# Kernel tuning notes

Hardware: AMD Instinct MI355X
Metric: run time of the kernel (lower is better)

Reference implementation:

```python
import jax, jax.numpy as jnp
import numpy as np

ALPHA, GAMMA = 0.25, 2.0            # focal loss params (cfg defaults)
W_CLASS, W_BBOX, W_GIOU = 2.0, 5.0, 2.0
N_CANDIDATE_K = 5                   # top-k ious used to derive dynamic k
CENTER_RADIUS = 2.5
B, Q, G, C = 32, 2000, 64, 80
IMG_W, IMG_H = 1333.0, 800.0


def _box_iou(a, b):
    # a: [Q,4] xyxy, b: [G,4] xyxy -> iou [Q,G], union [Q,G]
    area_a = (a[:, 2] - a[:, 0]) * (a[:, 3] - a[:, 1])
    area_b = (b[:, 2] - b[:, 0]) * (b[:, 3] - b[:, 1])
    lt = jnp.maximum(a[:, None, :2], b[None, :, :2])
    rb = jnp.minimum(a[:, None, 2:], b[None, :, 2:])
    wh = jnp.clip(rb - lt, 0.0)
    inter = wh[..., 0] * wh[..., 1]
    union = area_a[:, None] + area_b[None, :] - inter
    return inter / union, union


def _generalized_box_iou(a, b):
    iou, union = _box_iou(a, b)
    lt = jnp.minimum(a[:, None, :2], b[None, :, :2])
    rb = jnp.maximum(a[:, None, 2:], b[None, :, 2:])
    wh = jnp.clip(rb - lt, 0.0)
    area_c = wh[..., 0] * wh[..., 1]
    return iou - (area_c - union) / area_c


def _get_in_boxes_info(boxes, gt):
    # boxes, gt: absolute xyxy. Anchor centers inside gt box / inside center region.
    cx = (boxes[:, 0] + boxes[:, 2]) * 0.5
    cy = (boxes[:, 1] + boxes[:, 3]) * 0.5
    is_in_boxes = ((cx[:, None] > gt[None, :, 0]) & (cx[:, None] < gt[None, :, 2]) &
                   (cy[:, None] > gt[None, :, 1]) & (cy[:, None] < gt[None, :, 3]))
    gt_cx = (gt[:, 0] + gt[:, 2]) * 0.5
    gt_cy = (gt[:, 1] + gt[:, 3]) * 0.5
    gt_w = gt[:, 2] - gt[:, 0]
    gt_h = gt[:, 3] - gt[:, 1]
    is_in_centers = ((cx[:, None] > (gt_cx - CENTER_RADIUS * gt_w)[None, :]) &
                     (cx[:, None] < (gt_cx + CENTER_RADIUS * gt_w)[None, :]) &
                     (cy[:, None] > (gt_cy - CENTER_RADIUS * gt_h)[None, :]) &
                     (cy[:, None] < (gt_cy + CENTER_RADIUS * gt_h)[None, :]))
    fg_mask = is_in_boxes.any(1) | is_in_centers.any(1)
    return fg_mask, is_in_boxes & is_in_centers


def _dedup(cost, matching):
    # queries matched to >1 gt keep only their min-cost gt
    over = matching.sum(1) > 1
    keep = jax.nn.one_hot(jnp.argmin(cost, axis=1), cost.shape[1], dtype=matching.dtype)
    return jnp.where(over[:, None], keep, matching)


def _dynamic_k_matching(cost, ious):
    Qn, Gn = cost.shape
    topk_ious = jax.lax.top_k(ious.T, N_CANDIDATE_K)[0]              # [G,k]
    dynamic_ks = jnp.maximum(topk_ious.sum(1).astype(jnp.int32), 1)  # [G]
    # rank of each query within each gt's cost column (ascending)
    ranks = jnp.argsort(jnp.argsort(cost, axis=0), axis=0)
    matching = (ranks < dynamic_ks[None, :]).astype(cost.dtype)      # [Q,G]
    matching = _dedup(cost, matching)

    # ensure every gt gets >=1 query; bounded loop replaces data-dependent while
    def body(_, carry):
        cost_c, match_c = carry
        unmatched = match_c.sum(0) == 0                              # [G]
        any_un = unmatched.any()
        matched_q = match_c.sum(1) > 0
        cost_n = cost_c + jnp.where(matched_q, 1e5, 0.0)[:, None]
        add = jax.nn.one_hot(jnp.argmin(cost_n, axis=0), Qn, dtype=match_c.dtype).T
        match_n = jnp.maximum(match_c, add * unmatched[None, :].astype(match_c.dtype))
        match_n = _dedup(cost_n, match_n)
        return (jnp.where(any_un, cost_n, cost_c), jnp.where(any_un, match_n, match_c))

    cost, matching = jax.lax.fori_loop(0, Gn, body, (cost, matching))
    masked = jnp.where(matching > 0, cost, jnp.inf)
    matched_query_id = jnp.argmin(masked, axis=0)                    # [G]
    return matching, matched_query_id


def _match_one(logits, boxes, tgt_ids, gt_boxes, size_out, size_tgt):
    fg_mask, in_bc = _get_in_boxes_info(boxes, gt_boxes)
    ious, _ = _box_iou(boxes, gt_boxes)                              # [Q,G]
    neg = (1.0 - ALPHA) * logits ** GAMMA * (-jnp.log(1.0 - logits + 1e-8))
    pos = ALPHA * (1.0 - logits) ** GAMMA * (-jnp.log(logits + 1e-8))
    cost_class = jnp.take(pos - neg, tgt_ids, axis=1)                # [Q,G]
    out_n = boxes / size_out                                         # [Q,4]
    tgt_n = gt_boxes / size_tgt                                      # [G,4]
    cost_bbox = jnp.abs(out_n[:, None, :] - tgt_n[None, :, :]).sum(-1)  # L1 cdist
    cost_giou = -_generalized_box_iou(boxes, gt_boxes)
    cost = (W_BBOX * cost_bbox + W_CLASS * cost_class + W_GIOU * cost_giou
            + 100.0 * (~in_bc).astype(cost_bbox.dtype))
    cost = cost + jnp.where(fg_mask, 0.0, 1e4)[:, None]
    return _dynamic_k_matching(cost, ious)


def _rand_boxes(key, n_shape):
    k1, k2 = jax.random.split(key)
    wh = jnp.array([IMG_W, IMG_H], jnp.float32)
    ctr = jax.random.uniform(k1, n_shape + (2,)) * wh
    size = jax.random.uniform(k2, n_shape + (2,)) * (wh * 0.3) + 8.0
    x1y1 = jnp.clip(ctr - size * 0.5, 0.0, wh)
    x2y2 = jnp.clip(ctr + size * 0.5, 0.0, wh)
    x2y2 = jnp.maximum(x2y2, x1y1 + 1.0)
    return jnp.concatenate([x1y1, x2y2], axis=-1)


def setup_inputs() -> dict:
    key = jax.random.key(0)
    k1, k2, k3, k4 = jax.random.split(key, 4)
    pred_logits = jax.random.uniform(k1, (B, Q, C), minval=1e-4, maxval=1.0 - 1e-4)
    pred_boxes = _rand_boxes(k2, (B, Q))
    gt_classes = jax.random.randint(k3, (B, G), 0, C)
    gt_boxes = _rand_boxes(k4, (B, G))
    sz = jnp.array([IMG_W, IMG_H, IMG_W, IMG_H], jnp.float32)
    return {
        'pred_logits': pred_logits,
        'pred_boxes': pred_boxes,
        'gt_classes': gt_classes,
        'gt_boxes': gt_boxes,
        'image_size_xyxy': jnp.tile(sz, (B, 1)),
        'image_size_xyxy_tgt': jnp.tile(sz, (B, G, 1)),
    }


def reference(pred_logits, pred_boxes, gt_classes, gt_boxes, image_size_xyxy, image_size_xyxy_tgt):
    # matching: [B,Q,G] 0/1 assignment matrix (row q matched to gt g);
    # matched_query_id: [B,G] best query per gt. Padded-G, fixed-shape analog of
    # the per-image variable-length (indices, matched_ids) lists.
    matching, matched_query_id = jax.vmap(_match_one)(
        pred_logits, pred_boxes, gt_classes, gt_boxes, image_size_xyxy, image_size_xyxy_tgt)
    return matching, matched_query_id
```

## Files before the change

### kernel.cpp

```cpp
#include <hip/hip_runtime.h>
#include <cmath>

#pragma clang fp contract(off)

#define BB 32
#define QQ 2000
#define GG 64
#define CCH 80
#define TOPC 16

__global__ __launch_bounds__(256) void cost_kernel(
    const float* __restrict__ logits, const float* __restrict__ boxes,
    const int* __restrict__ gtc, const float* __restrict__ gtb,
    const float* __restrict__ szout, const float* __restrict__ sztgt,
    float* __restrict__ cost, int* __restrict__ rowarg) {
#pragma clang fp contract(off)
  const int b = blockIdx.y;
  const int q0 = blockIdx.x * 64;
  const int t = threadIdx.x;
  const int w = t >> 6, lane = t & 63;

  __shared__ float4 s_qb[64];
  __shared__ float s_tile[64 * 65];

  const int gbase = (b * GG + lane) * 4;
  const float g0 = gtb[gbase + 0], g1 = gtb[gbase + 1];
  const float g2 = gtb[gbase + 2], g3 = gtb[gbase + 3];
  const float t0 = g0 / sztgt[gbase + 0], t1 = g1 / sztgt[gbase + 1];
  const float t2 = g2 / sztgt[gbase + 2], t3 = g3 / sztgt[gbase + 3];
  const float garea = (g2 - g0) * (g3 - g1);
  const float gcx = (g0 + g2) * 0.5f, gcy = (g1 + g3) * 0.5f;
  const float gw = g2 - g0, gh = g3 - g1;
  const float cxlo = gcx - 2.5f * gw, cxhi = gcx + 2.5f * gw;
  const float cylo = gcy - 2.5f * gh, cyhi = gcy + 2.5f * gh;
  const int cls = gtc[b * GG + lane];
  const float so0 = szout[b * 4 + 0], so1 = szout[b * 4 + 1];
  const float so2 = szout[b * 4 + 2], so3 = szout[b * 4 + 3];

  if (t < 64) {
    int q = q0 + t;
    s_qb[t] = (q < QQ) ? reinterpret_cast<const float4*>(boxes)[b * QQ + q]
                       : make_float4(0.f, 0.f, 1.f, 1.f);
  }
  __syncthreads();

  const float* lbase = logits + (size_t)b * QQ * CCH;
  for (int i = 0; i < 16; ++i) {
    const int qi = w * 16 + i;
    const int q = q0 + qi;
    float4 bx = s_qb[qi];
    float x1 = bx.x, y1 = bx.y, x2 = bx.z, y2 = bx.w;
    float on0 = x1 / so0, on1 = y1 / so1, on2 = x2 / so2, on3 = y2 / so3;
    float cx = (x1 + x2) * 0.5f, cy = (y1 + y2) * 0.5f;
    float areaa = (x2 - x1) * (y2 - y1);

    bool ib = (cx > g0) & (cx < g2) & (cy > g1) & (cy < g3);
    bool ic = (cx > cxlo) & (cx < cxhi) & (cy > cylo) & (cy < cyhi);
    bool fg = (__ballot(ib) != 0ull) || (__ballot(ic) != 0ull);
    float fgadd = fg ? 0.0f : 1e4f;

    float ltx = fmaxf(x1, g0), lty = fmaxf(y1, g1);
    float rbx = fminf(x2, g2), rby = fminf(y2, g3);
    float iw = fmaxf(rbx - ltx, 0.0f), ih = fmaxf(rby - lty, 0.0f);
    float inter = iw * ih;
    float uni = (areaa + garea) - inter;
    float iou = inter / uni;
    float ex1 = fminf(x1, g0), ey1 = fminf(y1, g1);
    float ex2 = fmaxf(x2, g2), ey2 = fmaxf(y2, g3);
    float ew = fmaxf(ex2 - ex1, 0.0f), eh = fmaxf(ey2 - ey1, 0.0f);
    float areac = ew * eh;
    float giou = iou - (areac - uni) / areac;

    float p = (q < QQ) ? lbase[(size_t)q * CCH + cls] : 0.5f;
    float negc = (0.75f * (p * p)) * (-logf((1.0f - p) + 1e-8f));
    float posc = (0.25f * ((1.0f - p) * (1.0f - p))) * (-logf(p + 1e-8f));
    float ccls = posc - negc;

    float cb = ((fabsf(on0 - t0) + fabsf(on1 - t1)) + fabsf(on2 - t2)) + fabsf(on3 - t3);
    float notbc = (ib & ic) ? 0.0f : 1.0f;
    float c = ((5.0f * cb + 2.0f * ccls) + 2.0f * (-giou)) + 100.0f * notbc;
    c = c + fgadd;

    s_tile[qi * 65 + lane] = c;

    float bv = c; int bg = lane;
    for (int off = 32; off; off >>= 1) {
      float ov = __shfl_down(bv, off, 64); int og = __shfl_down(bg, off, 64);
      if (ov < bv || (ov == bv && og < bg)) { bv = ov; bg = og; }
    }
    if (lane == 0 && q < QQ) rowarg[b * QQ + q] = bg;
  }
  __syncthreads();

  float* cb_out = cost + (size_t)b * GG * QQ;
  const int qi = t & 63;
  const int q = q0 + qi;
  if (q < QQ) {
    #pragma unroll
    for (int pass = 0; pass < 16; ++pass) {
      int g = (t >> 6) + pass * 4;
      cb_out[(size_t)g * QQ + q] = s_tile[qi * 65 + g];
    }
  }
}

__global__ __launch_bounds__(256) void pick_kernel(
    const float* __restrict__ boxes, const float* __restrict__ gtb,
    const float* __restrict__ cost, short* __restrict__ lists,
    int* __restrict__ dynks) {
#pragma clang fp contract(off)
  const int gwave = blockIdx.x * 4 + (threadIdx.x >> 6);
  const int lane = threadIdx.x & 63;
  const int b = gwave >> 6, col = gwave & 63;

  const int gbase = (b * GG + col) * 4;
  const float gx1 = gtb[gbase + 0], gy1 = gtb[gbase + 1];
  const float gx2 = gtb[gbase + 2], gy2 = gtb[gbase + 3];
  const float ga = (gx2 - gx1) * (gy2 - gy1);

  float v[32];
  #pragma unroll
  for (int j = 0; j < 32; ++j) {
    int q = lane + (j << 6);
    if (q < QQ) {
      float4 bx = reinterpret_cast<const float4*>(boxes)[b * QQ + q];
      float areaa = (bx.z - bx.x) * (bx.w - bx.y);
      float ltx = fmaxf(bx.x, gx1), lty = fmaxf(bx.y, gy1);
      float rbx = fminf(bx.z, gx2), rby = fminf(bx.w, gy2);
      float iw = fmaxf(rbx - ltx, 0.0f), ih = fmaxf(rby - lty, 0.0f);
      float inter = iw * ih;
      v[j] = inter / ((areaa + ga) - inter);
    } else v[j] = -1.0f;
  }
  unsigned rm = 0u;
  float s = 0.0f;
  for (int pass = 0; pass < 5; ++pass) {
    float bv = -1e30f; int bq = 0x7fffffff;
    #pragma unroll
    for (int j = 0; j < 32; ++j) {
      int q = lane + (j << 6);
      if (q < QQ && !((rm >> j) & 1u) && v[j] > bv) { bv = v[j]; bq = q; }
    }
    for (int off = 32; off; off >>= 1) {
      float ov = __shfl_down(bv, off, 64); int oq = __shfl_down(bq, off, 64);
      if (ov > bv || (ov == bv && oq < bq)) { bv = ov; bq = oq; }
    }
    bv = __shfl(bv, 0, 64); bq = __shfl(bq, 0, 64);
    s += bv;
    if ((bq & 63) == lane) rm |= (1u << (bq >> 6));
  }
  int dynk = (int)s;
  if (dynk < 1) dynk = 1;
  if (lane == 0) dynks[b * GG + col] = dynk;

  const float* ccol = cost + (size_t)(b * GG + col) * QQ;
  #pragma unroll
  for (int j = 0; j < 32; ++j) {
    int q = lane + (j << 6);
    v[j] = (q < QQ) ? ccol[q] : 0.0f;
  }
  rm = 0u;
  for (int pass = 0; pass < TOPC; ++pass) {
    float bv = INFINITY; int bq = 0x7fffffff;
    #pragma unroll
    for (int j = 0; j < 32; ++j) {
      int q = lane + (j << 6);
      if (q < QQ && !((rm >> j) & 1u) && v[j] < bv) { bv = v[j]; bq = q; }
    }
    for (int off = 32; off; off >>= 1) {
      float ov = __shfl_down(bv, off, 64); int oq = __shfl_down(bq, off, 64);
      if (ov < bv || (ov == bv && oq < bq)) { bv = ov; bq = oq; }
    }
    bq = __shfl(bq, 0, 64);
    if (lane == 0) lists[(b * GG + col) * TOPC + pass] = (short)bq;
    if ((bq & 63) == lane) rm |= (1u << (bq >> 6));
  }
}

__global__ __launch_bounds__(256) void serial_kernel(
    const float* __restrict__ cost, const short* __restrict__ lists,
    const int* __restrict__ dynks, const int* __restrict__ rowarg,
    uint2* __restrict__ bits, float* __restrict__ out_ids) {
#pragma clang fp contract(off)
  const int b = blockIdx.x;
  const int tid = threadIdx.x;
  const int w = tid >> 6, lane = tid & 63;

  __shared__ unsigned s_mlo[QQ], s_mhi[QQ];
  __shared__ int s_first[QQ];
  __shared__ int s_pushed[QQ];
  __shared__ short s_rarg[QQ];
  __shared__ short s_list[GG * TOPC];
  __shared__ int s_cnt[GG];
  __shared__ short s_chosen[GG];
  __shared__ unsigned long long s_pack[GG];
  __shared__ int s_added[128];
  __shared__ unsigned s_gmlo, s_gmhi;
  __shared__ int s_anyun, s_nadd;

  for (int q = tid; q < QQ; q += 256) {
    s_mlo[q] = 0u; s_mhi[q] = 0u; s_first[q] = -1; s_pushed[q] = -1;
    s_rarg[q] = (short)rowarg[b * QQ + q];
  }
  for (int i = tid; i < GG * TOPC; i += 256) s_list[i] = lists[b * GG * TOPC + i];
  if (tid < GG) s_cnt[tid] = 0;
  __syncthreads();

  if (tid < GG) {
    int dynk = dynks[b * GG + tid];
    s_cnt[tid] = dynk;
    for (int i = 0; i < dynk; ++i) {
      int q = s_list[tid * TOPC + i];
      if (tid < 32) atomicOr(&s_mlo[q], 1u << tid);
      else          atomicOr(&s_mhi[q], 1u << (tid - 32));
      s_first[q] = 0;
    }
  }
  __syncthreads();

  for (int q = tid; q < QQ; q += 256) {
    unsigned lo = s_mlo[q], hi = s_mhi[q];
    if (__popc(lo) + __popc(hi) > 1) {
      int bg = s_rarg[q];
      unsigned tl = lo, th = hi;
      while (tl) { int g = __ffs(tl) - 1; tl &= tl - 1; if (g != bg) atomicSub(&s_cnt[g], 1); }
      while (th) { int g = __ffs(th) + 31; th &= th - 1; if (g != bg) atomicSub(&s_cnt[g], 1); }
      bool had = (bg < 32) ? ((lo >> bg) & 1u) : ((hi >> (bg - 32)) & 1u);
      if (!had) atomicAdd(&s_cnt[bg], 1);
      s_mlo[q] = (bg < 32) ? (1u << bg) : 0u;
      s_mhi[q] = (bg >= 32) ? (1u << (bg - 32)) : 0u;
    }
  }

  const float* costb = cost + (size_t)b * GG * QQ;
  int T = 0;
  for (int iter = 0; iter < GG; ++iter) {
    __syncthreads();
    if (tid < 64) {
      unsigned long long bal = __ballot(s_cnt[tid] > 0);
      if (tid == 0) {
        s_gmlo = (unsigned)bal; s_gmhi = (unsigned)(bal >> 32);
        s_anyun = ((~bal) != 0ull); s_nadd = 0;
      }
    }
    __syncthreads();
    if (!s_anyun) break;
    T++;
    const unsigned gmlo = s_gmlo, gmhi = s_gmhi;

    for (int col = w; col < GG; col += 4) {
      bool matched = (col < 32) ? ((gmlo >> col) & 1u) : ((gmhi >> (col - 32)) & 1u);
      if (matched) continue;
      int cq = s_list[col * TOPC + (lane & (TOPC - 1))];
      bool cand_un = (lane < TOPC) && ((s_mlo[cq] | s_mhi[cq]) == 0u);
      unsigned long long bal = __ballot(cand_un);
      int q;
      if (bal) {
        q = s_list[col * TOPC + (__ffsll(bal) - 1)];
      } else {
        const float* ccol = costb + (size_t)col * QQ;
        float bv = INFINITY; int bq = 0x7fffffff;
        for (int q2 = lane; q2 < QQ; q2 += 64) {
          if ((s_mlo[q2] | s_mhi[q2]) == 0u) {
            float cv = ccol[q2];
            if (cv < bv) { bv = cv; bq = q2; }
          }
        }
        for (int off = 32; off; off >>= 1) {
          float ov = __shfl_down(bv, off, 64); int oq = __shfl_down(bq, off, 64);
          if (ov < bv || (ov == bv && oq < bq)) { bv = ov; bq = oq; }
        }
        bq = __shfl(bq, 0, 64);
        if (bq == 0x7fffffff) {
          bv = INFINITY; bq = 0x7fffffff;
          for (int q2 = lane; q2 < QQ; q2 += 64) {
            float cv = ccol[q2];
            int k = (s_first[q2] >= 0) ? (iter + 1 - s_first[q2]) : 0;
            for (int tt = 0; tt < k; ++tt) cv += 1e5f;
            if (cv < bv) { bv = cv; bq = q2; }
          }
          for (int off = 32; off; off >>= 1) {
            float ov = __shfl_down(bv, off, 64); int oq = __shfl_down(bq, off, 64);
            if (ov < bv || (ov == bv && oq < bq)) { bv = ov; bq = oq; }
          }
          bq = __shfl(bq, 0, 64);
        }
        q = bq;
      }
      if (lane == 0) s_chosen[col] = (short)q;
    }
    __syncthreads();

    if (tid < 64) {
      bool matched = (tid < 32) ? ((gmlo >> tid) & 1u) : ((gmhi >> (tid - 32)) & 1u);
      if (!matched) {
        int q = s_chosen[tid];
        if (tid < 32) atomicOr(&s_mlo[q], 1u << tid);
        else          atomicOr(&s_mhi[q], 1u << (tid - 32));
        atomicAdd(&s_cnt[tid], 1);
        if (s_first[q] == -1) s_first[q] = iter + 1;
        if (atomicExch(&s_pushed[q], iter) != iter) {
          int slot = atomicAdd(&s_nadd, 1);
          s_added[slot] = q;
        }
      }
    }
    __syncthreads();

    if (tid < s_nadd) {
      int q = s_added[tid];
      unsigned lo = s_mlo[q], hi = s_mhi[q];
      if (__popc(lo) + __popc(hi) > 1) {
        int bg = s_rarg[q];
        unsigned tl = lo, th = hi;
        while (tl) { int g = __ffs(tl) - 1; tl &= tl - 1; if (g != bg) atomicSub(&s_cnt[g], 1); }
        while (th) { int g = __ffs(th) + 31; th &= th - 1; if (g != bg) atomicSub(&s_cnt[g], 1); }
        bool had = (bg < 32) ? ((lo >> bg) & 1u) : ((hi >> (bg - 32)) & 1u);
        if (!had) atomicAdd(&s_cnt[bg], 1);
        s_mlo[q] = (bg < 32) ? (1u << bg) : 0u;
        s_mhi[q] = (bg >= 32) ? (1u << (bg - 32)) : 0u;
      }
    }
  }

  if (tid < GG) s_pack[tid] = 0xFFFFFFFFFFFFFFFFull;
  __syncthreads();
  for (int q = tid; q < QQ; q += 256) {
    unsigned lo = s_mlo[q], hi = s_mhi[q];
    if (lo | hi) {
      int g = lo ? (__ffs(lo) - 1) : (__ffs(hi) + 31);
      float cv = costb[(size_t)g * QQ + q];
      int k = T - s_first[q];
      for (int tt = 0; tt < k; ++tt) cv += 1e5f;
      unsigned ub = __float_as_uint(cv);
      ub = (ub & 0x80000000u) ? ~ub : (ub | 0x80000000u);
      unsigned long long pk = ((unsigned long long)ub << 16) | (unsigned)q;
      atomicMin(&s_pack[g], pk);
    }
  }
  __syncthreads();
  if (tid < GG) {
    unsigned long long pk = s_pack[tid];
    out_ids[b * GG + tid] =
        (pk == 0xFFFFFFFFFFFFFFFFull) ? 0.0f : (float)(pk & 0xFFFFull);
  }
  for (int q = tid; q < QQ; q += 256) bits[b * QQ + q] = make_uint2(s_mlo[q], s_mhi[q]);
}

__global__ __launch_bounds__(256) void expand_kernel(
    const uint2* __restrict__ bits, float* __restrict__ out_match) {
  int idx = blockIdx.x * 256 + threadIdx.x;
  if (idx >= BB * QQ * 16) return;
  int g4 = idx & 15;
  int bq = idx >> 4;
  uint2 m = bits[bq];
  unsigned mm = (g4 < 8) ? m.x : m.y;
  int sh = (g4 * 4) & 31;
  float4 o;
  o.x = (float)((mm >> (sh + 0)) & 1u);
  o.y = (float)((mm >> (sh + 1)) & 1u);
  o.z = (float)((mm >> (sh + 2)) & 1u);
  o.w = (float)((mm >> (sh + 3)) & 1u);
  reinterpret_cast<float4*>(out_match)[idx] = o;
}

extern "C" void kernel_launch(void* const* d_in, const int* in_sizes, int n_in,
                              void* d_out, int out_size, void* d_ws, size_t ws_size,
                              hipStream_t stream) {
  const float* logits = (const float*)d_in[0];
  const float* boxes  = (const float*)d_in[1];
  const int*   gtc    = (const int*)d_in[2];
  const float* gtbx   = (const float*)d_in[3];
  const float* szout  = (const float*)d_in[4];
  const float* sztgt  = (const float*)d_in[5];
  float* out = (float*)d_out;

  const size_t costN   = (size_t)BB * GG * QQ;
  const size_t rowargN = (size_t)BB * QQ;
  const size_t listsN  = (size_t)BB * GG * TOPC;
  const size_t dynksN  = (size_t)BB * GG;
  const size_t bitsN   = (size_t)BB * QQ;

  char* wsb = (char*)d_ws;
  const size_t extras = rowargN * 4 + listsN * 2 + dynksN * 4 + bitsN * 8;
  float* cost; char* p;
  if (ws_size >= costN * 4 + extras) {
    cost = (float*)wsb;
    p = wsb + costN * 4;
  } else {
    cost = out;
    p = wsb;
  }
  int*   rowarg = (int*)p;            p += rowargN * 4;
  short* lists  = (short*)p;          p += listsN * 2;
  int*   dynks  = (int*)p;            p += dynksN * 4;
  uint2* bits   = (uint2*)p;

  float* out_ids = out + costN;

  hipLaunchKernelGGL(cost_kernel, dim3(32, BB), dim3(256), 0, stream,
                     logits, boxes, gtc, gtbx, szout, sztgt, cost, rowarg);
  hipLaunchKernelGGL(pick_kernel, dim3(BB * GG / 4), dim3(256), 0, stream,
                     boxes, gtbx, cost, lists, dynks);
  hipLaunchKernelGGL(serial_kernel, dim3(BB), dim3(256), 0, stream,
                     cost, lists, dynks, rowarg, bits, out_ids);
  hipLaunchKernelGGL(expand_kernel, dim3((BB * QQ * 16) / 256), dim3(256), 0, stream,
                     bits, out);
}
```

Before: 151.5 us.

## Run serial matching loop in a single wave and fuse output expansion

Moves the iterative dynamic-k matching loop onto one 64-lane wave, packing four unmatched columns per wave step with 16-lane subgroups. This removes the block-wide barriers on every iteration. The output matrix is now zeroed inside cost_kernel and the serial kernel scatters the ones directly, so expand_kernel and the bits buffer go away. The cost buffer is always placed in the workspace with no fallback to the output. The trade-off is less parallelism in the cost-column fallback scans, and the workspace must be large enough.

```diff
diff --git a/kernel.cpp b/kernel.cpp
--- a/kernel.cpp
+++ b/kernel.cpp
@@ -13,7 +13,8 @@
     const float* __restrict__ logits, const float* __restrict__ boxes,
     const int* __restrict__ gtc, const float* __restrict__ gtb,
     const float* __restrict__ szout, const float* __restrict__ sztgt,
-    float* __restrict__ cost, int* __restrict__ rowarg) {
+    float* __restrict__ cost, int* __restrict__ rowarg,
+    float* __restrict__ out_match) {
 #pragma clang fp contract(off)
   const int b = blockIdx.y;
   const int q0 = blockIdx.x * 64;
@@ -102,6 +103,14 @@
       cb_out[(size_t)g * QQ + q] = s_tile[qi * 65 + g];
     }
   }
+
+  int nq = QQ - q0; if (nq > 64) nq = 64;
+  if (nq > 0) {
+    float4* zb = reinterpret_cast<float4*>(out_match + ((size_t)b * QQ + q0) * GG);
+    int n4 = nq * GG / 4;
+    float4 z = make_float4(0.f, 0.f, 0.f, 0.f);
+    for (int i = t; i < n4; i += 256) zb[i] = z;
+  }
 }
 
 __global__ __launch_bounds__(256) void pick_kernel(
@@ -180,11 +189,10 @@
 __global__ __launch_bounds__(256) void serial_kernel(
     const float* __restrict__ cost, const short* __restrict__ lists,
     const int* __restrict__ dynks, const int* __restrict__ rowarg,
-    uint2* __restrict__ bits, float* __restrict__ out_ids) {
+    float* __restrict__ out_match, float* __restrict__ out_ids) {
 #pragma clang fp contract(off)
   const int b = blockIdx.x;
   const int tid = threadIdx.x;
-  const int w = tid >> 6, lane = tid & 63;
 
   __shared__ unsigned s_mlo[QQ], s_mhi[QQ];
   __shared__ int s_first[QQ];
@@ -194,9 +202,10 @@
   __shared__ int s_cnt[GG];
   __shared__ short s_chosen[GG];
   __shared__ unsigned long long s_pack[GG];
-  __shared__ int s_added[128];
-  __shared__ unsigned s_gmlo, s_gmhi;
-  __shared__ int s_anyun, s_nadd;
+  __shared__ int s_added[GG];
+  __shared__ short s_ucols[GG];
+  __shared__ short s_fb[GG];
+  __shared__ int s_nadd, s_nfb, s_Tv;
 
   for (int q = tid; q < QQ; q += 256) {
     s_mlo[q] = 0u; s_mhi[q] = 0u; s_first[q] = -1; s_pushed[q] = -1;
@@ -231,33 +240,49 @@
       s_mhi[q] = (bg >= 32) ? (1u << (bg - 32)) : 0u;
     }
   }
+  __syncthreads();
 
   const float* costb = cost + (size_t)b * GG * QQ;
-  int T = 0;
-  for (int iter = 0; iter < GG; ++iter) {
-    __syncthreads();
-    if (tid < 64) {
-      unsigned long long bal = __ballot(s_cnt[tid] > 0);
-      if (tid == 0) {
-        s_gmlo = (unsigned)bal; s_gmhi = (unsigned)(bal >> 32);
-        s_anyun = ((~bal) != 0ull); s_nadd = 0;
+
+  if (tid < 64) {
+    const int lane = tid;
+    int T = 0;
+    for (int iter = 0; iter < GG; ++iter) {
+      unsigned long long bal = __ballot(s_cnt[lane] > 0);
+      unsigned long long um = ~bal;
+      if (um == 0ull) break;
+      T++;
+
+      bool isun = (um >> lane) & 1ull;
+      int nu = __popcll(um);
+      int pos = __popcll(um & ((1ull << lane) - 1ull));
+      if (isun) s_ucols[pos] = (short)lane;
+      if (lane == 0) { s_nfb = 0; s_nadd = 0; }
+
+      const int sg = lane >> 4, li = lane & 15;
+      for (int base = 0; base < nu; base += 4) {
+        int ci = base + sg;
+        int col = (ci < nu) ? (int)s_ucols[ci] : -1;
+        bool cand_un = false; int cq = 0;
+        if (col >= 0) {
+          cq = s_list[col * TOPC + li];
+          cand_un = ((s_mlo[cq] | s_mhi[cq]) == 0u);
+        }
+        unsigned long long bb = __ballot(cand_un);
+        unsigned sub = (unsigned)((bb >> (sg * 16)) & 0xFFFFull);
+        if (col >= 0) {
+          if (sub) {
+            if (li == __ffs(sub) - 1) s_chosen[col] = (short)cq;
+          } else if (li == 0) {
+            int slot = atomicAdd(&s_nfb, 1);
+            s_fb[slot] = (short)col;
+          }
+        }
       }
-    }
-    __syncthreads();
-    if (!s_anyun) break;
-    T++;
-    const unsigned gmlo = s_gmlo, gmhi = s_gmhi;
-
-    for (int col = w; col < GG; col += 4) {
-      bool matched = (col < 32) ? ((gmlo >> col) & 1u) : ((gmhi >> (col - 32)) & 1u);
-      if (matched) continue;
-      int cq = s_list[col * TOPC + (lane & (TOPC - 1))];
-      bool cand_un = (lane < TOPC) && ((s_mlo[cq] | s_mhi[cq]) == 0u);
-      unsigned long long bal = __ballot(cand_un);
-      int q;
-      if (bal) {
-        q = s_list[col * TOPC + (__ffsll(bal) - 1)];
-      } else {
+
+      int nfb = s_nfb;
+      for (int fi = 0; fi < nfb; ++fi) {
+        int col = s_fb[fi];
         const float* ccol = costb + (size_t)col * QQ;
         float bv = INFINITY; int bq = 0x7fffffff;
         for (int q2 = lane; q2 < QQ; q2 += 64) {
@@ -285,43 +310,41 @@
           }
           bq = __shfl(bq, 0, 64);
         }
-        q = bq;
+        if (lane == 0) s_chosen[col] = (short)bq;
       }
-      if (lane == 0) s_chosen[col] = (short)q;
-    }
-    __syncthreads();
-
-    if (tid < 64) {
-      bool matched = (tid < 32) ? ((gmlo >> tid) & 1u) : ((gmhi >> (tid - 32)) & 1u);
-      if (!matched) {
-        int q = s_chosen[tid];
-        if (tid < 32) atomicOr(&s_mlo[q], 1u << tid);
-        else          atomicOr(&s_mhi[q], 1u << (tid - 32));
-        atomicAdd(&s_cnt[tid], 1);
+
+      if (isun) {
+        int q = s_chosen[lane];
+        if (lane < 32) atomicOr(&s_mlo[q], 1u << lane);
+        else           atomicOr(&s_mhi[q], 1u << (lane - 32));
+        atomicAdd(&s_cnt[lane], 1);
         if (s_first[q] == -1) s_first[q] = iter + 1;
         if (atomicExch(&s_pushed[q], iter) != iter) {
           int slot = atomicAdd(&s_nadd, 1);
           s_added[slot] = q;
         }
       }
-    }
-    __syncthreads();
-
-    if (tid < s_nadd) {
-      int q = s_added[tid];
-      unsigned lo = s_mlo[q], hi = s_mhi[q];
-      if (__popc(lo) + __popc(hi) > 1) {
-        int bg = s_rarg[q];
-        unsigned tl = lo, th = hi;
-        while (tl) { int g = __ffs(tl) - 1; tl &= tl - 1; if (g != bg) atomicSub(&s_cnt[g], 1); }
-        while (th) { int g = __ffs(th) + 31; th &= th - 1; if (g != bg) atomicSub(&s_cnt[g], 1); }
-        bool had = (bg < 32) ? ((lo >> bg) & 1u) : ((hi >> (bg - 32)) & 1u);
-        if (!had) atomicAdd(&s_cnt[bg], 1);
-        s_mlo[q] = (bg < 32) ? (1u << bg) : 0u;
-        s_mhi[q] = (bg >= 32) ? (1u << (bg - 32)) : 0u;
+
+      int na = s_nadd;
+      if (lane < na) {
+        int q = s_added[lane];
+        unsigned lo = s_mlo[q], hi = s_mhi[q];
+        if (__popc(lo) + __popc(hi) > 1) {
+          int bg = s_rarg[q];
+          unsigned tl = lo, th = hi;
+          while (tl) { int g = __ffs(tl) - 1; tl &= tl - 1; if (g != bg) atomicSub(&s_cnt[g], 1); }
+          while (th) { int g = __ffs(th) + 31; th &= th - 1; if (g != bg) atomicSub(&s_cnt[g], 1); }
+          bool had = (bg < 32) ? ((lo >> bg) & 1u) : ((hi >> (bg - 32)) & 1u);
+          if (!had) atomicAdd(&s_cnt[bg], 1);
+          s_mlo[q] = (bg < 32) ? (1u << bg) : 0u;
+          s_mhi[q] = (bg >= 32) ? (1u << (bg - 32)) : 0u;
+        }
       }
     }
-  }
+    if (tid == 0) s_Tv = T;
+  }
+  __syncthreads();
+  const int T = s_Tv;
 
   if (tid < GG) s_pack[tid] = 0xFFFFFFFFFFFFFFFFull;
   __syncthreads();
@@ -344,24 +367,13 @@
     out_ids[b * GG + tid] =
         (pk == 0xFFFFFFFFFFFFFFFFull) ? 0.0f : (float)(pk & 0xFFFFull);
   }
-  for (int q = tid; q < QQ; q += 256) bits[b * QQ + q] = make_uint2(s_mlo[q], s_mhi[q]);
-}
-
-__global__ __launch_bounds__(256) void expand_kernel(
-    const uint2* __restrict__ bits, float* __restrict__ out_match) {
-  int idx = blockIdx.x * 256 + threadIdx.x;
-  if (idx >= BB * QQ * 16) return;
-  int g4 = idx & 15;
-  int bq = idx >> 4;
-  uint2 m = bits[bq];
-  unsigned mm = (g4 < 8) ? m.x : m.y;
-  int sh = (g4 * 4) & 31;
-  float4 o;
-  o.x = (float)((mm >> (sh + 0)) & 1u);
-  o.y = (float)((mm >> (sh + 1)) & 1u);
-  o.z = (float)((mm >> (sh + 2)) & 1u);
-  o.w = (float)((mm >> (sh + 3)) & 1u);
-  reinterpret_cast<float4*>(out_match)[idx] = o;
+  for (int q = tid; q < QQ; q += 256) {
+    unsigned lo = s_mlo[q], hi = s_mhi[q];
+    if (lo | hi) {
+      int g = lo ? (__ffs(lo) - 1) : (__ffs(hi) + 31);
+      out_match[((size_t)b * QQ + q) * GG + g] = 1.0f;
+    }
+  }
 }
 
 extern "C" void kernel_launch(void* const* d_in, const int* in_sizes, int n_in,
@@ -375,35 +387,23 @@
   const float* sztgt  = (const float*)d_in[5];
   float* out = (float*)d_out;
 
-  const size_t costN   = (size_t)BB * GG * QQ;
+  const size_t matchN  = (size_t)BB * QQ * GG;
   const size_t rowargN = (size_t)BB * QQ;
   const size_t listsN  = (size_t)BB * GG * TOPC;
   const size_t dynksN  = (size_t)BB * GG;
-  const size_t bitsN   = (size_t)BB * QQ;
-
-  char* wsb = (char*)d_ws;
-  const size_t extras = rowargN * 4 + listsN * 2 + dynksN * 4 + bitsN * 8;
-  float* cost; char* p;
-  if (ws_size >= costN * 4 + extras) {
-    cost = (float*)wsb;
-    p = wsb + costN * 4;
-  } else {
-    cost = out;
-    p = wsb;
-  }
+
+  char* p = (char*)d_ws;
+  float* cost   = (float*)p;          p += matchN * 4;
   int*   rowarg = (int*)p;            p += rowargN * 4;
   short* lists  = (short*)p;          p += listsN * 2;
-  int*   dynks  = (int*)p;            p += dynksN * 4;
-  uint2* bits   = (uint2*)p;
-
-  float* out_ids = out + costN;
+  int*   dynks  = (int*)p;
+
+  float* out_ids = out + matchN;
 
   hipLaunchKernelGGL(cost_kernel, dim3(32, BB), dim3(256), 0, stream,
-                     logits, boxes, gtc, gtbx, szout, sztgt, cost, rowarg);
+                     logits, boxes, gtc, gtbx, szout, sztgt, cost, rowarg, out);
   hipLaunchKernelGGL(pick_kernel, dim3(BB * GG / 4), dim3(256), 0, stream,
                      boxes, gtbx, cost, lists, dynks);
   hipLaunchKernelGGL(serial_kernel, dim3(BB), dim3(256), 0, stream,
-                     cost, lists, dynks, rowarg, bits, out_ids);
-  hipLaunchKernelGGL(expand_kernel, dim3((BB * QQ * 16) / 256), dim3(256), 0, stream,
-                     bits, out);
+                     cost, lists, dynks, rowarg, out, out_ids);
 }
```

Measured after the change: 147.5 us. -2.6%, faster.
